# Optimization experiments

Hardware: AMD Instinct MI355X
Metric: run time of the kernel (lower is better)

## Reference

```python
import jax, jax.numpy as jnp
import numpy as np

T = 8192
D_IN = 64          # state_dim + action_dim = 48 + 16
H = 2048           # hidden_size
OUT = 49           # state_dim + 1


def _glorot(key, shape):
    # eqx.nn.Linear default init: uniform(-1/sqrt(in), 1/sqrt(in))
    lim = 1.0 / np.sqrt(shape[-1])
    return jax.random.uniform(key, shape, jnp.float32, -lim, lim)


def setup_inputs() -> dict:
    key = jax.random.key(0)
    ks = jax.random.split(key, 14)
    x = jax.random.normal(ks[0], (T, D_IN), jnp.float32)
    enc_w = _glorot(ks[1], (H, D_IN))
    enc_b = _glorot(ks[2], (H,))
    # GRUCell params (eqx layout: [3H, in]/[3H, H], gate order: reset, update, new)
    w_ih = _glorot(ks[3], (3 * H, H))
    w_hh = _glorot(ks[4], (3 * H, H))
    b_ih = _glorot(ks[5], (3 * H,))
    b_n = _glorot(ks[6], (H,))
    # MLP decoder: depth=2, width=H, relu activations, identity final
    mlp_w0 = _glorot(ks[7], (H, H))
    mlp_b0 = _glorot(ks[8], (H,))
    mlp_w1 = _glorot(ks[9], (H, H))
    mlp_b1 = _glorot(ks[10], (H,))
    mlp_w2 = _glorot(ks[11], (OUT, H))
    mlp_b2 = _glorot(ks[12], (OUT,))
    return {"x": x, "enc_w": enc_w, "enc_b": enc_b, "w_ih": w_ih, "w_hh": w_hh,
            "b_ih": b_ih, "b_n": b_n, "mlp_w0": mlp_w0, "mlp_b0": mlp_b0,
            "mlp_w1": mlp_w1, "mlp_b1": mlp_b1, "mlp_w2": mlp_w2, "mlp_b2": mlp_b2}


def reference(x, enc_w, enc_b, w_ih, w_hh, b_ih, b_n,
              mlp_w0, mlp_b0, mlp_w1, mlp_b1, mlp_w2, mlp_b2):
    # encode: vmapped Linear over time -> [T, H]
    xe = x @ enc_w.T + enc_b
    # input-side gate pre-activations for all steps (hoisted out of the scan)
    igates = (xe @ w_ih.T + b_ih).reshape(T, 3, H)  # [T, 3, H]

    def cell(h, ig):
        hg = (w_hh @ h).reshape(3, H)
        r = jax.nn.sigmoid(ig[0] + hg[0])            # reset gate
        z = jax.nn.sigmoid(ig[1] + hg[1])            # update gate
        n = jnp.tanh(ig[2] + r * (hg[2] + b_n))      # candidate
        h_new = n + z * (h - n)                      # eqx GRUCell update
        return h_new, h_new

    h0 = jnp.zeros((H,), x.dtype)
    _, hs = jax.lax.scan(cell, h0, igates)           # hs: [T, H]

    # decode: MLP(H -> OUT, width H, depth 2, relu)
    h = jax.nn.relu(hs @ mlp_w0.T + mlp_b0)
    h = jax.nn.relu(h @ mlp_w1.T + mlp_b1)
    outs = h @ mlp_w2.T + mlp_b2                     # [T, OUT]
    return outs
```

## Files before the change

### kernel.cpp

```cpp
#include <hip/hip_runtime.h>
#include <math.h>

#define T_STEPS 8192
#define HID 2048
#define H3 6144
#define NBLK 256
#define CHUNK 2048

typedef float f32x4 __attribute__((ext_vector_type(4)));

__device__ __forceinline__ float4 cload_f4(const float* p) {
    float4 r;
    asm volatile("global_load_dwordx4 %0, %1, off sc0 sc1\n\t"
                 "s_waitcnt vmcnt(0)"
                 : "=&v"(r) : "v"(p) : "memory");
    return r;
}
__device__ __forceinline__ void cstore_f4(float4* p, float x, float y,
                                          float z, float w) {
    f32x4 v; v[0] = x; v[1] = y; v[2] = z; v[3] = w;
    asm volatile("global_store_dwordx4 %0, %1, off sc0 sc1"
                 :: "v"(p), "v"(v) : "memory");
}

#define BAR_LDS() asm volatile("s_waitcnt lgkmcnt(0)\n\ts_barrier" ::: "memory")

__device__ __forceinline__ float fexp2(float x) {
    return __builtin_amdgcn_exp2f(x);
}
__device__ __forceinline__ float frcp(float x) { return __builtin_amdgcn_rcpf(x); }
__device__ __forceinline__ float fsigmoid(float x) {
    return frcp(1.f + fexp2(-1.44269504089f * x));
}
__device__ __forceinline__ float ftanh_(float x) {
    return 2.f * frcp(1.f + fexp2(-2.88539008178f * x)) - 1.f;
}

template<int RELU>
__global__ __launch_bounds__(256) void sgemm_bias(
    const float* __restrict__ A, const float* __restrict__ B,
    const float* __restrict__ bias, float* __restrict__ C,
    int M, int N, int K)
{
    __shared__ float As[16][64];
    __shared__ float Bs[16][64];
    const int tid = threadIdx.x;
    const int tm = tid & 15;
    const int tn = tid >> 4;
    const int m0 = blockIdx.y * 64;
    const int n0 = blockIdx.x * 64;
    const int lm = tid >> 2;
    const int lk = (tid & 3) * 4;

    float c[4][4] = {};

    for (int k0 = 0; k0 < K; k0 += 16) {
        float4 av = *(const float4*)(A + (size_t)(m0 + lm) * K + k0 + lk);
        float4 bv = make_float4(0.f, 0.f, 0.f, 0.f);
        const int bn = n0 + lm;
        if (bn < N) bv = *(const float4*)(B + (size_t)bn * K + k0 + lk);
        __syncthreads();
        As[lk+0][lm] = av.x; As[lk+1][lm] = av.y; As[lk+2][lm] = av.z; As[lk+3][lm] = av.w;
        Bs[lk+0][lm] = bv.x; Bs[lk+1][lm] = bv.y; Bs[lk+2][lm] = bv.z; Bs[lk+3][lm] = bv.w;
        __syncthreads();
        #pragma unroll
        for (int kk = 0; kk < 16; kk++) {
            float4 a4 = *(const float4*)&As[kk][tm * 4];
            float4 b4 = *(const float4*)&Bs[kk][tn * 4];
            c[0][0] += a4.x * b4.x; c[0][1] += a4.x * b4.y; c[0][2] += a4.x * b4.z; c[0][3] += a4.x * b4.w;
            c[1][0] += a4.y * b4.x; c[1][1] += a4.y * b4.y; c[1][2] += a4.y * b4.z; c[1][3] += a4.y * b4.w;
            c[2][0] += a4.z * b4.x; c[2][1] += a4.z * b4.y; c[2][2] += a4.z * b4.z; c[2][3] += a4.z * b4.w;
            c[3][0] += a4.w * b4.x; c[3][1] += a4.w * b4.y; c[3][2] += a4.w * b4.z; c[3][3] += a4.w * b4.w;
        }
    }

    const int mrow = m0 + tm * 4;
    #pragma unroll
    for (int i = 0; i < 4; i++) {
        #pragma unroll
        for (int j = 0; j < 4; j++) {
            const int n = n0 + tn * 4 + j;
            if (n < N) {
                float v = c[i][j] + bias[n];
                if (RELU) v = fmaxf(v, 0.f);
                C[(size_t)(mrow + i) * N + n] = v;
            }
        }
    }
}

__global__ __launch_bounds__(256) void sgemm_nn(
    const float* __restrict__ A, const float* __restrict__ B,
    float* __restrict__ C, int M, int N, int K)
{
    __shared__ float As[16][64];
    __shared__ float Bs[16][64];
    const int tid = threadIdx.x;
    const int tm = tid & 15;
    const int tn = tid >> 4;
    const int m0 = blockIdx.y * 64;
    const int n0 = blockIdx.x * 64;
    const int lm = tid >> 2;
    const int lk = (tid & 3) * 4;
    const int bk  = tid >> 4;
    const int bn4 = (tid & 15) * 4;

    float c[4][4] = {};

    for (int k0 = 0; k0 < K; k0 += 16) {
        float4 av = *(const float4*)(A + (size_t)(m0 + lm) * K + k0 + lk);
        float4 bv = *(const float4*)(B + (size_t)(k0 + bk) * N + n0 + bn4);
        __syncthreads();
        As[lk+0][lm] = av.x; As[lk+1][lm] = av.y; As[lk+2][lm] = av.z; As[lk+3][lm] = av.w;
        *(float4*)&Bs[bk][bn4] = bv;
        __syncthreads();
        #pragma unroll
        for (int kk = 0; kk < 16; kk++) {
            float4 a4 = *(const float4*)&As[kk][tm * 4];
            float4 b4 = *(const float4*)&Bs[kk][tn * 4];
            c[0][0] += a4.x * b4.x; c[0][1] += a4.x * b4.y; c[0][2] += a4.x * b4.z; c[0][3] += a4.x * b4.w;
            c[1][0] += a4.y * b4.x; c[1][1] += a4.y * b4.y; c[1][2] += a4.y * b4.z; c[1][3] += a4.y * b4.w;
            c[2][0] += a4.z * b4.x; c[2][1] += a4.z * b4.y; c[2][2] += a4.z * b4.z; c[2][3] += a4.z * b4.w;
            c[3][0] += a4.w * b4.x; c[3][1] += a4.w * b4.y; c[3][2] += a4.w * b4.z; c[3][3] += a4.w * b4.w;
        }
    }

    const int mrow = m0 + tm * 4;
    #pragma unroll
    for (int i = 0; i < 4; i++) {
        #pragma unroll
        for (int j = 0; j < 4; j++)
            C[(size_t)(mrow + i) * N + n0 + tn * 4 + j] = c[i][j];
    }
}

__global__ __launch_bounds__(256) void bcomb_kernel(
    const float* __restrict__ w_ih, const float* __restrict__ enc_b,
    const float* __restrict__ b_ih, float* __restrict__ b_comb)
{
    const int wv = threadIdx.x >> 6, lane = threadIdx.x & 63;
    const int r = blockIdx.x * 4 + wv;
    const float* row = w_ih + (size_t)r * HID;
    float acc = 0.f;
    for (int j = lane; j < HID; j += 64) acc += row[j] * enc_b[j];
    #pragma unroll
    for (int m = 32; m >= 1; m >>= 1) acc += __shfl_xor(acc, m, 64);
    if (lane == 0) b_comb[r] = acc + b_ih[r];
}

__global__ __launch_bounds__(1024, 4) void gru_scan(
    const float* __restrict__ w_hh, const float* __restrict__ b_n,
    const float* __restrict__ ig,
    float* __restrict__ hs,
    float4* __restrict__ atoms,
    int base, int steps)
{
    __shared__ float h_lds[HID];
    __shared__ float pg[16][3];
    __shared__ float hg_lds[24];
    const int tid  = threadIdx.x;
    const int lane = tid & 63;
    const int w    = tid >> 6;
    const int pr   = tid & 127;
    const int k    = tid >> 7;
    const int b    = blockIdx.x;

    float4 wreg[3][4];
    #pragma unroll
    for (int j = 0; j < 3; j++) {
        const int idx3 = 3 * k + j;
        const float* wp = w_hh +
            (size_t)((idx3 >> 3) * HID + b * 8 + (idx3 & 7)) * HID;
        #pragma unroll
        for (int m = 0; m < 4; m++)
            wreg[j][m] = *(const float4*)(wp + 4 * pr + 512 * m);
    }

    const int i = b * 8 + tid;
    const float bn = (tid < 8) ? b_n[i] : 0.f;

    for (int t = 0; t < steps; t++) {
        float ig0 = 0.f, ig1 = 0.f, ig2 = 0.f;
        if (tid < 8) {
            const float* p = ig + (size_t)t * H3 + i;
            ig0 = p[0]; ig1 = p[HID]; ig2 = p[2 * HID];
        }

        const float target = (float)(base + t);
        const float* ap = (const float*)(atoms + (t & 1) * 1024 + tid);
        float4 f;
        do { f = cload_f4(ap); } while (f.z < target);
        *(float2*)&h_lds[2 * tid] = make_float2(f.x, f.y);
        BAR_LDS();

        float a0 = 0.f, a1 = 0.f, a2 = 0.f;
        #pragma unroll
        for (int m = 0; m < 4; m++) {
            float4 h4 = *(const float4*)&h_lds[4 * pr + 512 * m];
            a0 += wreg[0][m].x * h4.x + wreg[0][m].y * h4.y + wreg[0][m].z * h4.z + wreg[0][m].w * h4.w;
            a1 += wreg[1][m].x * h4.x + wreg[1][m].y * h4.y + wreg[1][m].z * h4.z + wreg[1][m].w * h4.w;
            a2 += wreg[2][m].x * h4.x + wreg[2][m].y * h4.y + wreg[2][m].z * h4.z + wreg[2][m].w * h4.w;
        }
        #pragma unroll
        for (int s = 32; s >= 1; s >>= 1) {
            a0 += __shfl_xor(a0, s, 64);
            a1 += __shfl_xor(a1, s, 64);
            a2 += __shfl_xor(a2, s, 64);
        }
        if (lane == 0) { pg[w][0] = a0; pg[w][1] = a1; pg[w][2] = a2; }
        BAR_LDS();

        if (w == 0) {
            if (lane < 24) {
                const int kk = lane / 3, j = lane - 3 * kk;
                hg_lds[lane] = pg[2 * kk][j] + pg[2 * kk + 1][j];
            }
            asm volatile("s_waitcnt lgkmcnt(0)" ::: "memory");
            float h_new = 0.f;
            if (lane < 8) {
                const float r = fsigmoid(ig0 + hg_lds[lane]);
                const float z = fsigmoid(ig1 + hg_lds[8 + lane]);
                const float n = ftanh_(ig2 + r * (hg_lds[16 + lane] + bn));
                const float hp = h_lds[i];
                h_new = n + z * (hp - n);
            }
            const float ha = __shfl(h_new, lane * 2, 64);
            const float hb = __shfl(h_new, lane * 2 + 1, 64);
            if (lane < 4) {
                cstore_f4(atoms + ((t + 1) & 1) * 1024 + b * 4 + lane,
                          ha, hb, (float)(base + t + 1), 0.f);
            }
            if (lane < 8)
                hs[(size_t)t * HID + i] = h_new;
        }
    }
}

extern "C" void kernel_launch(void* const* d_in, const int* in_sizes, int n_in,
                              void* d_out, int out_size, void* d_ws, size_t ws_size,
                              hipStream_t stream) {
    const float* x     = (const float*)d_in[0];
    const float* enc_w = (const float*)d_in[1];
    const float* enc_b = (const float*)d_in[2];
    const float* w_ih  = (const float*)d_in[3];
    const float* w_hh  = (const float*)d_in[4];
    const float* b_ih  = (const float*)d_in[5];
    const float* b_n   = (const float*)d_in[6];
    const float* w0    = (const float*)d_in[7];
    const float* b0    = (const float*)d_in[8];
    const float* w1    = (const float*)d_in[9];
    const float* b1    = (const float*)d_in[10];
    const float* w2    = (const float*)d_in[11];
    const float* b2    = (const float*)d_in[12];
    float* out = (float*)d_out;

    float* R1    = (float*)d_ws;
    float* R2    = R1 + (size_t)16777216;
    float* wcomb = R2 + (size_t)16777216;
    float* bcomb = wcomb + 393216;
    float4* atoms = (float4*)(bcomb + 6144);

    (void)hipMemsetAsync(atoms, 0, 2 * 1024 * sizeof(float4), stream);

    sgemm_nn<<<dim3(1, 96), 256, 0, stream>>>(w_ih, enc_w, wcomb, 6144, 64, 2048);
    bcomb_kernel<<<dim3(1536), 256, 0, stream>>>(w_ih, enc_b, b_ih, bcomb);

    for (int c = 0; c < T_STEPS / CHUNK; c++) {
        sgemm_bias<0><<<dim3(H3 / 64, CHUNK / 64), 256, 0, stream>>>(
            x + (size_t)c * CHUNK * 64, wcomb, bcomb, R1, CHUNK, H3, 64);
        gru_scan<<<dim3(NBLK), dim3(1024), 0, stream>>>(
            w_hh, b_n, R1, R2 + (size_t)c * CHUNK * HID, atoms, c * CHUNK, CHUNK);
    }

    sgemm_bias<1><<<dim3(HID / 64, T_STEPS / 64), 256, 0, stream>>>(
        R2, w0, b0, R1, T_STEPS, HID, HID);
    sgemm_bias<1><<<dim3(HID / 64, T_STEPS / 64), 256, 0, stream>>>(
        R1, w1, b1, R2, T_STEPS, HID, HID);
    sgemm_bias<0><<<dim3(1, T_STEPS / 64), 256, 0, stream>>>(
        R2, w2, b2, out, T_STEPS, 49, 2048);
}
```

Baseline: 25.81 ms.

## Relay per-step hidden-state polling through an elected leader block per XCD

Each block reads its XCD id and elects one leader block per XCD per chunk. Only the leader spins on the global atoms buffer with system-coherent loads, then republishes the data to a per-XCD relay buffer using stores scoped to the local L2. The other blocks poll that relay with cheaper L2-scoped loads and fall back to the global atoms after repeated misses. The goal is to cut cross-die coherent polling traffic on the serial GRU critical path. The cost is an extra relay hop and reliance on undocumented hwreg XCD-id semantics for correctness.

```diff
diff --git a/kernel.cpp b/kernel.cpp
--- a/kernel.cpp
+++ b/kernel.cpp
@@ -16,10 +16,23 @@
                  : "=&v"(r) : "v"(p) : "memory");
     return r;
 }
+__device__ __forceinline__ float4 cload_f4_l(const float* p) {
+    float4 r;
+    asm volatile("global_load_dwordx4 %0, %1, off sc0\n\t"
+                 "s_waitcnt vmcnt(0)"
+                 : "=&v"(r) : "v"(p) : "memory");
+    return r;
+}
 __device__ __forceinline__ void cstore_f4(float4* p, float x, float y,
                                           float z, float w) {
     f32x4 v; v[0] = x; v[1] = y; v[2] = z; v[3] = w;
     asm volatile("global_store_dwordx4 %0, %1, off sc0 sc1"
+                 :: "v"(p), "v"(v) : "memory");
+}
+__device__ __forceinline__ void cstore_f4_l(float4* p, float x, float y,
+                                            float z, float w) {
+    f32x4 v; v[0] = x; v[1] = y; v[2] = z; v[3] = w;
+    asm volatile("global_store_dwordx4 %0, %1, off sc0"
                  :: "v"(p), "v"(v) : "memory");
 }
 
@@ -153,11 +166,14 @@
     const float* __restrict__ ig,
     float* __restrict__ hs,
     float4* __restrict__ atoms,
+    float4* __restrict__ relay,
+    int* __restrict__ elect,
     int base, int steps)
 {
     __shared__ float h_lds[HID];
     __shared__ float pg[16][3];
     __shared__ float hg_lds[24];
+    __shared__ int lead_s, xcd_s;
     const int tid  = threadIdx.x;
     const int lane = tid & 63;
     const int w    = tid >> 6;
@@ -165,6 +181,18 @@
     const int k    = tid >> 7;
     const int b    = blockIdx.x;
 
+    if (tid == 0) {
+        int xcd;
+        asm volatile("s_getreg_b32 %0, hwreg(20, 0, 32)" : "=s"(xcd));
+        xcd &= 7;
+        xcd_s  = xcd;
+        lead_s = (atomicAdd(elect + (base / CHUNK) * 8 + xcd, 1) == 0) ? 1 : 0;
+    }
+    __syncthreads();
+    const int  xcd    = xcd_s;
+    const bool leader = (lead_s != 0);
+    float4* rbase = relay + (size_t)xcd * 2048;
+
     float4 wreg[3][4];
     #pragma unroll
     for (int j = 0; j < 3; j++) {
@@ -188,8 +216,24 @@
 
         const float target = (float)(base + t);
         const float* ap = (const float*)(atoms + (t & 1) * 1024 + tid);
+        float4* rp = rbase + (t & 1) * 1024 + tid;
         float4 f;
-        do { f = cload_f4(ap); } while (f.z < target);
+        if (leader) {
+            f = cload_f4(ap);
+            while (f.z < target) f = cload_f4(ap);
+            cstore_f4_l(rp, f.x, f.y, f.z, 0.f);
+        } else {
+            int miss = 0;
+            for (;;) {
+                f = cload_f4_l((const float*)rp);
+                if (f.z >= target) break;
+                if (++miss >= 32) {
+                    f = cload_f4(ap);
+                    if (f.z >= target) break;
+                    miss = 16;
+                }
+            }
+        }
         *(float2*)&h_lds[2 * tid] = make_float2(f.x, f.y);
         BAR_LDS();
 
@@ -259,8 +303,12 @@
     float* wcomb = R2 + (size_t)16777216;
     float* bcomb = wcomb + 393216;
     float4* atoms = (float4*)(bcomb + 6144);
+    float4* relay = (float4*)(R1 + (size_t)13000000);
+    int*    elect = (int*)(relay + 8 * 2048);
 
     (void)hipMemsetAsync(atoms, 0, 2 * 1024 * sizeof(float4), stream);
+    (void)hipMemsetAsync(relay, 0, 8 * 2048 * sizeof(float4) + 32 * sizeof(int),
+                         stream);
 
     sgemm_nn<<<dim3(1, 96), 256, 0, stream>>>(w_ih, enc_w, wcomb, 6144, 64, 2048);
     bcomb_kernel<<<dim3(1536), 256, 0, stream>>>(w_ih, enc_b, b_ih, bcomb);
@@ -269,7 +317,8 @@
         sgemm_bias<0><<<dim3(H3 / 64, CHUNK / 64), 256, 0, stream>>>(
             x + (size_t)c * CHUNK * 64, wcomb, bcomb, R1, CHUNK, H3, 64);
         gru_scan<<<dim3(NBLK), dim3(1024), 0, stream>>>(
-            w_hh, b_n, R1, R2 + (size_t)c * CHUNK * HID, atoms, c * CHUNK, CHUNK);
+            w_hh, b_n, R1, R2 + (size_t)c * CHUNK * HID, atoms, relay, elect,
+            c * CHUNK, CHUNK);
     }
 
     sgemm_bias<1><<<dim3(HID / 64, T_STEPS / 64), 256, 0, stream>>>(
```

New measurement: 72.09 ms. 2.79x slower.
